# Kernel tuning notes

Hardware: AMD Instinct MI355X
Metric: run time of the kernel (lower is better)

Reference implementation:

```python
import jax, jax.numpy as jnp
import numpy as np

N_NODES = 100000


def setup_inputs() -> dict:
    key = jax.random.key(0)
    k1, k2, k3, k4 = jax.random.split(key, 4)
    d = 64
    E = 1200000
    x = jax.random.normal(k1, (N_NODES, d), dtype=jnp.float32)
    edge_index = jax.random.randint(k2, (2, E), 0, N_NODES, dtype=jnp.int64)
    # GraphConv(dim, 1): lin_rel (with bias) applied to aggregated neighbors,
    # lin_root (no bias) applied to self features.
    W_rel = jax.random.normal(k3, (d, 1), dtype=jnp.float32) / np.sqrt(d)
    b_rel = jnp.zeros((1,), dtype=jnp.float32)
    W_root = jax.random.normal(k4, (d, 1), dtype=jnp.float32) / np.sqrt(d)
    return {"x": x, "edge_index": edge_index, "W_rel": W_rel, "b_rel": b_rel, "W_root": W_root}


def reference(x, edge_index, W_rel, b_rel, W_root):
    # x: [N, d], edge_index: [2, E] (row 0 = source j, row 1 = target i)
    src, dst = edge_index[0], edge_index[1]
    # sum-aggregate neighbor features: agg[i] = sum_{j: (j,i) in E} x[j]
    agg = jax.ops.segment_sum(x[src], dst, num_segments=N_NODES)  # [N, d]
    # GraphConv: lin_rel(agg) + lin_root(x) -> scalar score per node
    attn = agg @ W_rel + b_rel + x @ W_root  # [N, 1]
    return attn
```

## Files before the change

### kernel.cpp

```cpp
#include <hip/hip_runtime.h>

#define DIM 64
#define NPB 256
#define NPB_SHIFT 8
#define THREADS 512
#define K2_U 8
#define K2_EPB (THREADS * K2_U)
#define STRIP K2_EPB
#define SRC_BITS 17
#define SRC_MASK ((1u << SRC_BITS) - 1u)
#define NODE_ROWS 160

__global__ __launch_bounds__(THREADS)
void fused_kernel(const float4* __restrict__ x4,
                  const float4* __restrict__ Wrel4,
                  const float* __restrict__ b_rel,
                  const float4* __restrict__ Wroot4,
                  const int* __restrict__ ei,
                  float* __restrict__ s,
                  float* __restrict__ out,
                  unsigned* __restrict__ bucket,
                  unsigned short* __restrict__ offsT,
                  int E, int NB, int NBLK, int n) {
    __shared__ __align__(16) unsigned lpair[K2_EPB];
    __shared__ int  hist[THREADS];
    __shared__ int  wsum[8];

    int tid = threadIdx.x;

    if (blockIdx.x < NBLK) {
        int blk = blockIdx.x;
        hist[tid] = 0;
        __syncthreads();

        int base = blk * K2_EPB + tid * K2_U;
        int dst[K2_U], src[K2_U], rnk[K2_U], bin[K2_U];
        int have = 0;

        if (base + K2_U <= E) {
            const int4* sv = (const int4*)ei;
            const int4* dv = (const int4*)(ei + E);
            int g = base >> 2;
            int4 s0 = sv[g], s1 = sv[g + 1];
            int4 d0 = dv[g], d1 = dv[g + 1];
            src[0] = s0.x; src[1] = s0.y; src[2] = s0.z; src[3] = s0.w;
            src[4] = s1.x; src[5] = s1.y; src[6] = s1.z; src[7] = s1.w;
            dst[0] = d0.x; dst[1] = d0.y; dst[2] = d0.z; dst[3] = d0.w;
            dst[4] = d1.x; dst[5] = d1.y; dst[6] = d1.z; dst[7] = d1.w;
            have = K2_U;
        } else {
            #pragma unroll
            for (int k = 0; k < K2_U; ++k) {
                int e = base + k;
                if (e < E) {
                    src[k] = ei[e];
                    dst[k] = ei[E + e];
                    have = k + 1;
                }
            }
        }

        #pragma unroll
        for (int k = 0; k < K2_U; ++k) {
            if (k < have) {
                bin[k] = dst[k] >> NPB_SHIFT;
                rnk[k] = atomicAdd(&hist[bin[k]], 1);
            }
        }
        __syncthreads();

        int h = hist[tid];

        int lane = tid & 63;
        int w = tid >> 6;
        int incl = h;
        #pragma unroll
        for (int off = 1; off < 64; off <<= 1) {
            int v = __shfl_up(incl, off);
            if (lane >= off) incl += v;
        }
        if (lane == 63) wsum[w] = incl;
        __syncthreads();

        int wb = 0;
        #pragma unroll
        for (int i = 0; i < 8; ++i) wb += (i < w) ? wsum[i] : 0;
        int excl = wb + incl - h;

        if (tid <= NB)
            offsT[(size_t)tid * NBLK + blk] = (unsigned short)excl;

        hist[tid] = excl;
        __syncthreads();

        #pragma unroll
        for (int k = 0; k < K2_U; ++k) {
            if (k < have) {
                int slot = hist[bin[k]] + rnk[k];
                lpair[slot] = ((unsigned)(dst[k] & (NPB - 1)) << SRC_BITS)
                              | (unsigned)src[k];
            }
        }
        __syncthreads();

        int nE = min(K2_EPB, E - blk * K2_EPB);
        int n4 = (nE + 3) >> 2;
        const uint4* lp4 = (const uint4*)lpair;
        uint4* dp4 = (uint4*)(bucket + (size_t)blk * STRIP);
        for (int i = tid; i < n4; i += THREADS) dp4[i] = lp4[i];
    } else {
        int nb = blockIdx.x - NBLK;
        int lane16 = tid & 15;
        int rg = tid >> 4;
        int rowbase = nb * NODE_ROWS + rg;
        float4 wr = Wrel4[lane16];
        float4 wt = Wroot4[lane16];
        float b0 = b_rel[0];

        float4 xv[5];
        int row[5];
        #pragma unroll
        for (int k = 0; k < 5; ++k) {
            row[k] = rowbase + k * 32;
            xv[k] = (row[k] < n) ? x4[(size_t)row[k] * (DIM / 4) + lane16]
                                 : make_float4(0.f, 0.f, 0.f, 0.f);
        }
        #pragma unroll
        for (int k = 0; k < 5; ++k) {
            float sr = xv[k].x * wr.x + xv[k].y * wr.y
                     + xv[k].z * wr.z + xv[k].w * wr.w;
            float st = xv[k].x * wt.x + xv[k].y * wt.y
                     + xv[k].z * wt.z + xv[k].w * wt.w;
            #pragma unroll
            for (int off = 1; off < 16; off <<= 1) {
                sr += __shfl_xor(sr, off);
                st += __shfl_xor(st, off);
            }
            if (lane16 == 0 && row[k] < n) {
                s[row[k]]   = sr;
                out[row[k]] = st + b0;
            }
        }
    }
}

__global__ __launch_bounds__(THREADS)
void gather_kernel(const unsigned short* __restrict__ offsT,
                   const unsigned* __restrict__ bucket,
                   const float* __restrict__ s,
                   float* __restrict__ out,
                   int NB, int NBLK, int n) {
    __shared__ float acc[NPB];
    __shared__ unsigned short o0s[THREADS], o1s[THREADS];
    int b = blockIdx.x;
    int tid = threadIdx.x;

    if (tid < NPB) acc[tid] = 0.f;
    for (int t = tid; t < NBLK; t += THREADS) {
        o0s[t] = offsT[(size_t)b * NBLK + t];
        o1s[t] = offsT[(size_t)(b + 1) * NBLK + t];
    }
    __syncthreads();

    if (tid < NBLK) {
        int o0 = o0s[tid];
        int o1 = o1s[tid];
        const unsigned* sp = bucket + (size_t)tid * STRIP;
        int i = o0;
        for (; i < o1 && (i & 3); ++i) {
            unsigned p = sp[i];
            atomicAdd(&acc[p >> SRC_BITS], s[p & SRC_MASK]);
        }
        for (; i + 4 <= o1; i += 4) {
            uint4 q = *(const uint4*)(sp + i);
            float v0 = s[q.x & SRC_MASK];
            float v1 = s[q.y & SRC_MASK];
            float v2 = s[q.z & SRC_MASK];
            float v3 = s[q.w & SRC_MASK];
            atomicAdd(&acc[q.x >> SRC_BITS], v0);
            atomicAdd(&acc[q.y >> SRC_BITS], v1);
            atomicAdd(&acc[q.z >> SRC_BITS], v2);
            atomicAdd(&acc[q.w >> SRC_BITS], v3);
        }
        for (; i < o1; ++i) {
            unsigned p = sp[i];
            atomicAdd(&acc[p >> SRC_BITS], s[p & SRC_MASK]);
        }
    }
    __syncthreads();

    if (tid < NPB) {
        int g = b * NPB + tid;
        if (g < n) out[g] += acc[tid];
    }
}

extern "C" void kernel_launch(void* const* d_in, const int* in_sizes, int n_in,
                              void* d_out, int out_size, void* d_ws, size_t ws_size,
                              hipStream_t stream) {
    const float* x      = (const float*)d_in[0];
    const int*   ei     = (const int*)d_in[1];
    const float* W_rel  = (const float*)d_in[2];
    const float* b_rel  = (const float*)d_in[3];
    const float* W_root = (const float*)d_in[4];
    float* out = (float*)d_out;

    int n = out_size;
    int E = in_sizes[1] / 2;

    int NB   = (n + NPB - 1) / NPB;
    int NBLK = (E + K2_EPB - 1) / K2_EPB;

    float* s = (float*)d_ws;
    size_t off = ((size_t)n * 4 + 255) & ~(size_t)255;
    unsigned short* offsT = (unsigned short*)((char*)d_ws + off);
    off += ((size_t)(NB + 1) * NBLK * 2 + 255) & ~(size_t)255;
    unsigned* bucket = (unsigned*)((char*)d_ws + off);

    int NODEBLKS = (n + NODE_ROWS - 1) / NODE_ROWS;
    fused_kernel<<<NBLK + NODEBLKS, THREADS, 0, stream>>>(
        (const float4*)x, (const float4*)W_rel, b_rel, (const float4*)W_root,
        ei, s, out, bucket, offsT, E, NB, NBLK, n);

    gather_kernel<<<NB, THREADS, 0, stream>>>(offsT, bucket, s, out, NB, NBLK, n);
}
```

Measured before the change: 28.45 us.

## Pre-gather source scores during binning and pack truncated floats into bucket entries

Splits the fused kernel into separate node, bin and gather kernels so the bin pass can read the per-node scores s[src] directly. Each bucket entry now stores the 8-bit local destination plus a truncated 24-bit float value instead of a source index, so the gather kernel no longer does random reads of s. Edges per binning block are halved and gather loops over strips to handle more blocks. This adds a kernel launch and serialization, and drops 8 mantissa bits of each score, reducing accuracy.

```diff
diff --git a/kernel.cpp b/kernel.cpp
--- a/kernel.cpp
+++ b/kernel.cpp
@@ -4,154 +4,151 @@
 #define NPB 256
 #define NPB_SHIFT 8
 #define THREADS 512
-#define K2_U 8
+#define K2_U 4
 #define K2_EPB (THREADS * K2_U)
 #define STRIP K2_EPB
-#define SRC_BITS 17
-#define SRC_MASK ((1u << SRC_BITS) - 1u)
 #define NODE_ROWS 160
 
 __global__ __launch_bounds__(THREADS)
-void fused_kernel(const float4* __restrict__ x4,
-                  const float4* __restrict__ Wrel4,
-                  const float* __restrict__ b_rel,
-                  const float4* __restrict__ Wroot4,
-                  const int* __restrict__ ei,
-                  float* __restrict__ s,
-                  float* __restrict__ out,
-                  unsigned* __restrict__ bucket,
-                  unsigned short* __restrict__ offsT,
-                  int E, int NB, int NBLK, int n) {
+void node_kernel(const float4* __restrict__ x4,
+                 const float4* __restrict__ Wrel4,
+                 const float* __restrict__ b_rel,
+                 const float4* __restrict__ Wroot4,
+                 float* __restrict__ s,
+                 float* __restrict__ out,
+                 int n) {
+    int tid = threadIdx.x;
+    int lane16 = tid & 15;
+    int rg = tid >> 4;
+    int rowbase = blockIdx.x * NODE_ROWS + rg;
+    float4 wr = Wrel4[lane16];
+    float4 wt = Wroot4[lane16];
+    float b0 = b_rel[0];
+
+    float4 xv[5];
+    int row[5];
+    #pragma unroll
+    for (int k = 0; k < 5; ++k) {
+        row[k] = rowbase + k * 32;
+        xv[k] = (row[k] < n) ? x4[(size_t)row[k] * (DIM / 4) + lane16]
+                             : make_float4(0.f, 0.f, 0.f, 0.f);
+    }
+    #pragma unroll
+    for (int k = 0; k < 5; ++k) {
+        float sr = xv[k].x * wr.x + xv[k].y * wr.y
+                 + xv[k].z * wr.z + xv[k].w * wr.w;
+        float st = xv[k].x * wt.x + xv[k].y * wt.y
+                 + xv[k].z * wt.z + xv[k].w * wt.w;
+        #pragma unroll
+        for (int off = 1; off < 16; off <<= 1) {
+            sr += __shfl_xor(sr, off);
+            st += __shfl_xor(st, off);
+        }
+        if (lane16 == 0 && row[k] < n) {
+            s[row[k]]   = sr;
+            out[row[k]] = st + b0;
+        }
+    }
+}
+
+__global__ __launch_bounds__(THREADS)
+void bin_kernel(const int* __restrict__ ei,
+                const float* __restrict__ s,
+                unsigned* __restrict__ bucket,
+                unsigned short* __restrict__ offsT,
+                int E, int NB, int NBLK) {
     __shared__ __align__(16) unsigned lpair[K2_EPB];
     __shared__ int  hist[THREADS];
     __shared__ int  wsum[8];
 
     int tid = threadIdx.x;
-
-    if (blockIdx.x < NBLK) {
-        int blk = blockIdx.x;
-        hist[tid] = 0;
-        __syncthreads();
-
-        int base = blk * K2_EPB + tid * K2_U;
-        int dst[K2_U], src[K2_U], rnk[K2_U], bin[K2_U];
-        int have = 0;
-
-        if (base + K2_U <= E) {
-            const int4* sv = (const int4*)ei;
-            const int4* dv = (const int4*)(ei + E);
-            int g = base >> 2;
-            int4 s0 = sv[g], s1 = sv[g + 1];
-            int4 d0 = dv[g], d1 = dv[g + 1];
-            src[0] = s0.x; src[1] = s0.y; src[2] = s0.z; src[3] = s0.w;
-            src[4] = s1.x; src[5] = s1.y; src[6] = s1.z; src[7] = s1.w;
-            dst[0] = d0.x; dst[1] = d0.y; dst[2] = d0.z; dst[3] = d0.w;
-            dst[4] = d1.x; dst[5] = d1.y; dst[6] = d1.z; dst[7] = d1.w;
-            have = K2_U;
-        } else {
-            #pragma unroll
-            for (int k = 0; k < K2_U; ++k) {
-                int e = base + k;
-                if (e < E) {
-                    src[k] = ei[e];
-                    dst[k] = ei[E + e];
-                    have = k + 1;
-                }
-            }
-        }
-
+    int blk = blockIdx.x;
+    hist[tid] = 0;
+    __syncthreads();
+
+    int base = blk * K2_EPB + tid * K2_U;
+    int dst[K2_U], rnk[K2_U], bin[K2_U];
+    float val[K2_U];
+    int have = 0;
+
+    if (base + K2_U <= E) {
+        const int4* sv = (const int4*)ei;
+        const int4* dv = (const int4*)(ei + E);
+        int g = base >> 2;
+        int4 s0 = sv[g];
+        int4 d0 = dv[g];
+        val[0] = s[s0.x]; val[1] = s[s0.y]; val[2] = s[s0.z]; val[3] = s[s0.w];
+        dst[0] = d0.x; dst[1] = d0.y; dst[2] = d0.z; dst[3] = d0.w;
+        have = K2_U;
+    } else {
         #pragma unroll
         for (int k = 0; k < K2_U; ++k) {
-            if (k < have) {
-                bin[k] = dst[k] >> NPB_SHIFT;
-                rnk[k] = atomicAdd(&hist[bin[k]], 1);
+            int e = base + k;
+            if (e < E) {
+                val[k] = s[ei[e]];
+                dst[k] = ei[E + e];
+                have = k + 1;
             }
         }
-        __syncthreads();
-
-        int h = hist[tid];
-
-        int lane = tid & 63;
-        int w = tid >> 6;
-        int incl = h;
-        #pragma unroll
-        for (int off = 1; off < 64; off <<= 1) {
-            int v = __shfl_up(incl, off);
-            if (lane >= off) incl += v;
-        }
-        if (lane == 63) wsum[w] = incl;
-        __syncthreads();
-
-        int wb = 0;
-        #pragma unroll
-        for (int i = 0; i < 8; ++i) wb += (i < w) ? wsum[i] : 0;
-        int excl = wb + incl - h;
-
-        if (tid <= NB)
-            offsT[(size_t)tid * NBLK + blk] = (unsigned short)excl;
-
-        hist[tid] = excl;
-        __syncthreads();
-
-        #pragma unroll
-        for (int k = 0; k < K2_U; ++k) {
-            if (k < have) {
-                int slot = hist[bin[k]] + rnk[k];
-                lpair[slot] = ((unsigned)(dst[k] & (NPB - 1)) << SRC_BITS)
-                              | (unsigned)src[k];
-            }
-        }
-        __syncthreads();
-
-        int nE = min(K2_EPB, E - blk * K2_EPB);
-        int n4 = (nE + 3) >> 2;
-        const uint4* lp4 = (const uint4*)lpair;
-        uint4* dp4 = (uint4*)(bucket + (size_t)blk * STRIP);
-        for (int i = tid; i < n4; i += THREADS) dp4[i] = lp4[i];
-    } else {
-        int nb = blockIdx.x - NBLK;
-        int lane16 = tid & 15;
-        int rg = tid >> 4;
-        int rowbase = nb * NODE_ROWS + rg;
-        float4 wr = Wrel4[lane16];
-        float4 wt = Wroot4[lane16];
-        float b0 = b_rel[0];
-
-        float4 xv[5];
-        int row[5];
-        #pragma unroll
-        for (int k = 0; k < 5; ++k) {
-            row[k] = rowbase + k * 32;
-            xv[k] = (row[k] < n) ? x4[(size_t)row[k] * (DIM / 4) + lane16]
-                                 : make_float4(0.f, 0.f, 0.f, 0.f);
-        }
-        #pragma unroll
-        for (int k = 0; k < 5; ++k) {
-            float sr = xv[k].x * wr.x + xv[k].y * wr.y
-                     + xv[k].z * wr.z + xv[k].w * wr.w;
-            float st = xv[k].x * wt.x + xv[k].y * wt.y
-                     + xv[k].z * wt.z + xv[k].w * wt.w;
-            #pragma unroll
-            for (int off = 1; off < 16; off <<= 1) {
-                sr += __shfl_xor(sr, off);
-                st += __shfl_xor(st, off);
-            }
-            if (lane16 == 0 && row[k] < n) {
-                s[row[k]]   = sr;
-                out[row[k]] = st + b0;
-            }
-        }
-    }
+    }
+
+    #pragma unroll
+    for (int k = 0; k < K2_U; ++k) {
+        if (k < have) {
+            bin[k] = dst[k] >> NPB_SHIFT;
+            rnk[k] = atomicAdd(&hist[bin[k]], 1);
+        }
+    }
+    __syncthreads();
+
+    int h = hist[tid];
+
+    int lane = tid & 63;
+    int w = tid >> 6;
+    int incl = h;
+    #pragma unroll
+    for (int off = 1; off < 64; off <<= 1) {
+        int v = __shfl_up(incl, off);
+        if (lane >= off) incl += v;
+    }
+    if (lane == 63) wsum[w] = incl;
+    __syncthreads();
+
+    int wb = 0;
+    #pragma unroll
+    for (int i = 0; i < 8; ++i) wb += (i < w) ? wsum[i] : 0;
+    int excl = wb + incl - h;
+
+    if (tid <= NB)
+        offsT[(size_t)tid * NBLK + blk] = (unsigned short)excl;
+
+    hist[tid] = excl;
+    __syncthreads();
+
+    #pragma unroll
+    for (int k = 0; k < K2_U; ++k) {
+        if (k < have) {
+            int slot = hist[bin[k]] + rnk[k];
+            unsigned bits = __float_as_uint(val[k]);
+            lpair[slot] = ((unsigned)(dst[k] & (NPB - 1)) << 24) | (bits >> 8);
+        }
+    }
+    __syncthreads();
+
+    int nE = min(K2_EPB, E - blk * K2_EPB);
+    int n4 = (nE + 3) >> 2;
+    const uint4* lp4 = (const uint4*)lpair;
+    uint4* dp4 = (uint4*)(bucket + (size_t)blk * STRIP);
+    for (int i = tid; i < n4; i += THREADS) dp4[i] = lp4[i];
 }
 
 __global__ __launch_bounds__(THREADS)
 void gather_kernel(const unsigned short* __restrict__ offsT,
                    const unsigned* __restrict__ bucket,
-                   const float* __restrict__ s,
                    float* __restrict__ out,
                    int NB, int NBLK, int n) {
     __shared__ float acc[NPB];
-    __shared__ unsigned short o0s[THREADS], o1s[THREADS];
+    __shared__ unsigned short o0s[640], o1s[640];
     int b = blockIdx.x;
     int tid = threadIdx.x;
 
@@ -162,29 +159,25 @@
     }
     __syncthreads();
 
-    if (tid < NBLK) {
-        int o0 = o0s[tid];
-        int o1 = o1s[tid];
-        const unsigned* sp = bucket + (size_t)tid * STRIP;
+    for (int st = tid; st < NBLK; st += THREADS) {
+        int o0 = o0s[st];
+        int o1 = o1s[st];
+        const unsigned* sp = bucket + (size_t)st * STRIP;
         int i = o0;
         for (; i < o1 && (i & 3); ++i) {
             unsigned p = sp[i];
-            atomicAdd(&acc[p >> SRC_BITS], s[p & SRC_MASK]);
+            atomicAdd(&acc[p >> 24], __uint_as_float(p << 8));
         }
         for (; i + 4 <= o1; i += 4) {
             uint4 q = *(const uint4*)(sp + i);
-            float v0 = s[q.x & SRC_MASK];
-            float v1 = s[q.y & SRC_MASK];
-            float v2 = s[q.z & SRC_MASK];
-            float v3 = s[q.w & SRC_MASK];
-            atomicAdd(&acc[q.x >> SRC_BITS], v0);
-            atomicAdd(&acc[q.y >> SRC_BITS], v1);
-            atomicAdd(&acc[q.z >> SRC_BITS], v2);
-            atomicAdd(&acc[q.w >> SRC_BITS], v3);
+            atomicAdd(&acc[q.x >> 24], __uint_as_float(q.x << 8));
+            atomicAdd(&acc[q.y >> 24], __uint_as_float(q.y << 8));
+            atomicAdd(&acc[q.z >> 24], __uint_as_float(q.z << 8));
+            atomicAdd(&acc[q.w >> 24], __uint_as_float(q.w << 8));
         }
         for (; i < o1; ++i) {
             unsigned p = sp[i];
-            atomicAdd(&acc[p >> SRC_BITS], s[p & SRC_MASK]);
+            atomicAdd(&acc[p >> 24], __uint_as_float(p << 8));
         }
     }
     __syncthreads();
@@ -218,9 +211,11 @@
     unsigned* bucket = (unsigned*)((char*)d_ws + off);
 
     int NODEBLKS = (n + NODE_ROWS - 1) / NODE_ROWS;
-    fused_kernel<<<NBLK + NODEBLKS, THREADS, 0, stream>>>(
+    node_kernel<<<NODEBLKS, THREADS, 0, stream>>>(
         (const float4*)x, (const float4*)W_rel, b_rel, (const float4*)W_root,
-        ei, s, out, bucket, offsT, E, NB, NBLK, n);
-
-    gather_kernel<<<NB, THREADS, 0, stream>>>(offsT, bucket, s, out, NB, NBLK, n);
-}
+        s, out, n);
+
+    bin_kernel<<<NBLK, THREADS, 0, stream>>>(ei, s, bucket, offsT, E, NB, NBLK);
+
+    gather_kernel<<<NB, THREADS, 0, stream>>>(offsT, bucket, out, NB, NBLK, n);
+}
```

New measurement: 36.73 us. 1.29x slower.
